# Optimization experiments

Hardware: AMD Instinct MI355X
Metric: run time of the kernel (lower is better)

The kernel has to match this reference:

```python
import jax, jax.numpy as jnp
import numpy as np

B, S, D, H, DH, TLEN, TD = 4, 1024, 1024, 16, 64, 256, 256
EPS = 1e-5


def layer_norm(x, g, b):
    m = jnp.mean(x, axis=-1, keepdims=True)
    v = jnp.mean((x - m) ** 2, axis=-1, keepdims=True)
    return (x - m) * jax.lax.rsqrt(v + EPS) * g + b


def rotate_half(x):
    x1, x2 = jnp.split(x, 2, axis=-1)
    return jnp.concatenate((-x2, x1), axis=-1)


def apply_rope(pos, t):
    # pos: [S, DH] -> [1, S, 1, DH]; t: [B, S, H, DH]
    p = pos[None, :, None, :]
    return t * jnp.cos(p) + rotate_half(t) * jnp.sin(p)


def mha(q_in, kv_in, in_w, in_b, out_w, out_b, n_heads):
    # standard nn.MultiheadAttention math (batch-first tensors here)
    d = q_in.shape[-1]
    dh = d // n_heads
    q = q_in @ in_w[:d].T + in_b[:d]
    k = kv_in @ in_w[d:2 * d].T + in_b[d:2 * d]
    v = kv_in @ in_w[2 * d:].T + in_b[2 * d:]
    q = q.reshape(q.shape[0], q.shape[1], n_heads, dh)
    k = k.reshape(k.shape[0], k.shape[1], n_heads, dh)
    v = v.reshape(v.shape[0], v.shape[1], n_heads, dh)
    scores = jnp.einsum('bihd,bjhd->bhij', q, k) / jnp.sqrt(jnp.asarray(dh, q.dtype))
    attn = jax.nn.softmax(scores, axis=-1)
    o = jnp.einsum('bhij,bjhd->bihd', attn, v)
    o = o.reshape(o.shape[0], o.shape[1], d)
    return o @ out_w.T + out_b


def setup_inputs():
    key = jax.random.key(0)
    ks = jax.random.split(key, 20)
    s = 0.02
    inp = {
        'x': jax.random.normal(ks[0], (B, S, D), jnp.float32),
        'text_emb': jax.random.normal(ks[1], (B, TLEN, D), jnp.float32),
        'time_emb': jax.random.normal(ks[2], (B, TD), jnp.float32),
    }
    # true RoPE position encoding, matching RotaryEmbedding.forward
    inv_freq = 1.0 / (10000 ** (jnp.arange(0, DH, 2, dtype=jnp.float32) / DH))
    freqs = jnp.arange(S, dtype=jnp.float32)[:, None] * inv_freq[None, :]
    inp['rotary_pos'] = jnp.concatenate((freqs, freqs), axis=-1)  # [S, DH]
    inp.update(
        ln1_g=jnp.ones((D,), jnp.float32), ln1_b=jnp.zeros((D,), jnp.float32),
        ln2_g=jnp.ones((D,), jnp.float32), ln2_b=jnp.zeros((D,), jnp.float32),
        ln3_g=jnp.ones((D,), jnp.float32), ln3_b=jnp.zeros((D,), jnp.float32),
        attn_in_w=jax.random.normal(ks[3], (3 * D, D), jnp.float32) * s,
        attn_in_b=jnp.zeros((3 * D,), jnp.float32),
        ca_in_w=jax.random.normal(ks[4], (3 * D, D), jnp.float32) * s,
        ca_in_b=jnp.zeros((3 * D,), jnp.float32),
        ca_out_w=jax.random.normal(ks[5], (D, D), jnp.float32) * s,
        ca_out_b=jnp.zeros((D,), jnp.float32),
        fc1_w=jax.random.normal(ks[6], (4 * D, D), jnp.float32) * s,
        fc1_b=jnp.zeros((4 * D,), jnp.float32),
        gate_w=jax.random.normal(ks[7], (4 * D, D), jnp.float32) * s,
        gate_b=jnp.zeros((4 * D,), jnp.float32),
        fc2_w=jax.random.normal(ks[8], (D, 4 * D), jnp.float32) * s,
        fc2_b=jnp.zeros((D,), jnp.float32),
    )
    return inp


def reference(x, text_emb, time_emb, rotary_pos,
              ln1_g, ln1_b, ln2_g, ln2_b, ln3_g, ln3_b,
              attn_in_w, attn_in_b,
              ca_in_w, ca_in_b, ca_out_w, ca_out_b,
              fc1_w, fc1_b, gate_w, gate_b, fc2_w, fc2_b):
    b, n, d = x.shape
    # --- self-attention with manual RoPE (NOTE: original skips out_proj) ---
    residual = x
    xn = layer_norm(x, ln1_g, ln1_b)
    q = xn @ attn_in_w[:d].T + attn_in_b[:d]
    k = xn @ attn_in_w[d:2 * d].T + attn_in_b[d:2 * d]
    v = xn @ attn_in_w[2 * d:].T + attn_in_b[2 * d:]
    q = q.reshape(b, n, H, DH)
    k = k.reshape(b, n, H, DH)
    v = v.reshape(b, n, H, DH)
    q = apply_rope(rotary_pos, q)
    k = apply_rope(rotary_pos, k)
    scores = jnp.einsum('bihd,bjhd->bhij', q, k) / jnp.sqrt(jnp.asarray(DH, x.dtype))
    attn = jax.nn.softmax(scores, axis=-1)
    attn_out = jnp.einsum('bhij,bjhd->bihd', attn, v).reshape(b, n, d)
    x = attn_out + residual
    # --- cross-attention (full MHA, dropout inactive at eval) ---
    residual = x
    xn = layer_norm(x, ln2_g, ln2_b)
    x = mha(xn, text_emb, ca_in_w, ca_in_b, ca_out_w, ca_out_b, H) + residual
    # --- gated MLP ---
    residual = x
    xn = layer_norm(x, ln3_g, ln3_b)
    h = jax.nn.gelu(xn @ fc1_w.T + fc1_b, approximate=False)
    g = jax.nn.sigmoid(xn @ gate_w.T + gate_b)
    return (h * g) @ fc2_w.T + fc2_b + residual
```

## Files before the change

kernel.cpp:

```cpp
#include <hip/hip_runtime.h>
#include <hip/hip_bf16.h>

#define SEQ 1024
#define DIM 1024
#define NH 16

typedef __bf16 bf16_t;
typedef __bf16 bf16x8 __attribute__((ext_vector_type(8)));
typedef __bf16 bf16x4 __attribute__((ext_vector_type(4)));
typedef float f32x4 __attribute__((ext_vector_type(4)));

__device__ __forceinline__ f32x4 mfma16(bf16x8 a, bf16x8 b, f32x4 c) {
    return __builtin_amdgcn_mfma_f32_16x16x32_bf16(a, b, c, 0, 0, 0);
}

__device__ __forceinline__ void gload16(const bf16_t* g, bf16_t* l) {
    __builtin_amdgcn_global_load_lds(
        (const __attribute__((address_space(1))) void*)g,
        (__attribute__((address_space(3))) void*)l, 16, 0, 0);
}

enum { EPI_BF16 = 0, EPI_F32_RESID = 1, EPI_BF16_GELU = 2, EPI_BF16_SIGMUL = 3 };

__global__ __launch_bounds__(256) void cvt_kernel(const float* __restrict__ in,
                                                  bf16_t* __restrict__ out) {
    const int i = blockIdx.x * 256 + threadIdx.x;
    const float4 v = ((const float4*)in)[i];
    bf16x4 o = {(bf16_t)v.x, (bf16_t)v.y, (bf16_t)v.z, (bf16_t)v.w};
    ((bf16x4*)out)[i] = o;
}

__global__ __launch_bounds__(256) void ln_kernel(const float* __restrict__ in,
                                                 const float* __restrict__ g,
                                                 const float* __restrict__ bsh,
                                                 bf16_t* __restrict__ out) {
    __shared__ float red[4], red2[4];
    const int row = blockIdx.x, tid = threadIdx.x;
    const float4 v = ((const float4*)(in + (size_t)row * DIM))[tid];
    float s = v.x + v.y + v.z + v.w;
#pragma unroll
    for (int o = 32; o; o >>= 1) s += __shfl_down(s, o, 64);
    if ((tid & 63) == 0) red[tid >> 6] = s;
    __syncthreads();
    const float mean = (red[0] + red[1] + red[2] + red[3]) * (1.0f / DIM);
    const float dx = v.x - mean, dy = v.y - mean, dz = v.z - mean, dw = v.w - mean;
    float s2 = dx * dx + dy * dy + dz * dz + dw * dw;
#pragma unroll
    for (int o = 32; o; o >>= 1) s2 += __shfl_xor(s2, o, 64);
    if ((tid & 63) == 0) red2[tid >> 6] = s2;
    __syncthreads();
    const float var = (red2[0] + red2[1] + red2[2] + red2[3]) * (1.0f / DIM);
    const float rs = rsqrtf(var + 1e-5f);
    const float4 gv = ((const float4*)g)[tid];
    const float4 bv = ((const float4*)bsh)[tid];
    bf16x4 o4 = {(bf16_t)(dx * rs * gv.x + bv.x), (bf16_t)(dy * rs * gv.y + bv.y),
                 (bf16_t)(dz * rs * gv.z + bv.z), (bf16_t)(dw * rs * gv.w + bv.w)};
    ((bf16x4*)(out + (size_t)row * DIM))[tid] = o4;
}

__global__ __launch_bounds__(256) void rope_kernel(bf16_t* __restrict__ qkv,
                                                   const float* __restrict__ rp) {
    const int t = blockIdx.x * 256 + threadIdx.x;
    const int row = t >> 9;
    const int rem = t & 511;
    const int h = rem >> 5, d = rem & 31;
    const int s = row & (SEQ - 1);
    const float p0 = rp[s * 64 + d];
    const float p1 = rp[s * 64 + d + 32];
    float s0, c0, s1, c1;
    sincosf(p0, &s0, &c0);
    sincosf(p1, &s1, &c1);
    const size_t base = (size_t)row * 3072 + h * 64 + d;
#pragma unroll
    for (int off = 0; off <= 1024; off += 1024) {
        const float a = (float)qkv[base + off];
        const float b = (float)qkv[base + off + 32];
        qkv[base + off] = (bf16_t)(a * c0 - b * s0);
        qkv[base + off + 32] = (bf16_t)(b * c1 + a * s1);
    }
}

__device__ __forceinline__ float epi_apply_gelu(float v) {
    return 0.5f * v * (1.0f + erff(v * 0.70710678118f));
}

__global__ __launch_bounds__(256) void vtrans_kernel(
    const bf16_t* __restrict__ src, int ld, int voff, int skv,
    bf16_t* __restrict__ vt) {
    __shared__ bf16_t T[64 * 72];
    const int qt = blockIdx.x, h = blockIdx.y, b = blockIdx.z;
    const int tid = threadIdx.x;
    const int s0 = qt * 64;
#pragma unroll
    for (int t = 0; t < 2; ++t) {
        const int idx = t * 256 + tid;
        const int r = idx >> 3, c8 = (idx & 7) * 8;
        bf16x8 v = *(const bf16x8*)(src + (size_t)(b * skv + s0 + r) * ld +
                                    voff + h * 64 + c8);
        *(bf16x8*)&T[r * 72 + c8] = v;
    }
    __syncthreads();
    const size_t base = ((size_t)(b * NH + h) * 64) * skv;
#pragma unroll
    for (int t = 0; t < 2; ++t) {
        const int idx = t * 256 + tid;
        const int d = idx >> 3, s8 = (idx & 7) * 8;
        bf16x8 w;
#pragma unroll
        for (int i = 0; i < 8; ++i) w[i] = T[(s8 + i) * 72 + d];
        *(bf16x8*)(vt + base + (size_t)d * skv + s0 + s8) = w;
    }
}

#define ALD 72
template <bool OUTBF>
__global__ __launch_bounds__(256) void attn2_kernel(
    const bf16_t* __restrict__ qp, int ldq, int qoff,
    const bf16_t* __restrict__ kp, int ldk, int koff,
    const bf16_t* __restrict__ vtp, int skv,
    const float* __restrict__ resid, void* __restrict__ outp, float scale) {
    __shared__ bf16_t Ks[4096];
    __shared__ bf16_t Vs[4096];
    __shared__ bf16_t Ps[4 * 16 * ALD];
    const int nwg = gridDim.x;
    const int t = (blockIdx.x & 7) * (nwg >> 3) + (blockIdx.x >> 3);
    const int qt = t & 15;
    const int bh = t >> 4;
    const int b = bh >> 4, h = bh & 15;
    const int tid = threadIdx.x;
    const int wave = tid >> 6, lane = tid & 63;
    const int lr = lane & 15, hi = lane >> 4;

    const size_t qrow = (size_t)(b * SEQ + qt * 64 + wave * 16 + lr);
    const bf16_t* qb = qp + qrow * ldq + qoff + h * 64;
    const bf16x8 qf0 = *(const bf16x8*)(qb + hi * 8);
    const bf16x8 qf1 = *(const bf16x8*)(qb + 32 + hi * 8);

    const bf16_t* vbase = vtp + ((size_t)bh * 64) * skv;

    f32x4 oacc[4];
#pragma unroll
    for (int n = 0; n < 4; ++n) oacc[n] = (f32x4){0.f, 0.f, 0.f, 0.f};
    float mrun[4] = {-1e30f, -1e30f, -1e30f, -1e30f};
    float lrun[4] = {0.f, 0.f, 0.f, 0.f};

    bf16_t* pw = &Ps[wave * 16 * ALD];
    const int nkt = skv >> 6;
    for (int kt = 0; kt < nkt; ++kt) {
#pragma unroll
        for (int u = 0; u < 2; ++u) {
            const int c = wave * 2 + u;
            const int grow = wave * 16 + lr, gcol = u * 32 + hi * 8;
            gload16(kp + (size_t)(b * skv + kt * 64 + grow) * ldk + koff +
                        h * 64 + gcol,
                    &Ks[c * 512]);
            gload16(vbase + (size_t)grow * skv + kt * 64 + gcol, &Vs[c * 512]);
        }
        __syncthreads();

        f32x4 s[4];
#pragma unroll
        for (int n = 0; n < 4; ++n) {
            f32x4 z = (f32x4){0.f, 0.f, 0.f, 0.f};
            z = mfma16(qf0, *(const bf16x8*)&Ks[(n * 2 + 0) * 512 + hi * 128 + lr * 8], z);
            z = mfma16(qf1, *(const bf16x8*)&Ks[(n * 2 + 1) * 512 + hi * 128 + lr * 8], z);
            s[n] = z * scale;
        }
        float alpha[4];
#pragma unroll
        for (int j = 0; j < 4; ++j) {
            float mt = fmaxf(fmaxf(s[0][j], s[1][j]), fmaxf(s[2][j], s[3][j]));
#pragma unroll
            for (int o = 8; o >= 1; o >>= 1) mt = fmaxf(mt, __shfl_xor(mt, o, 64));
            const float mnew = fmaxf(mrun[j], mt);
            alpha[j] = __expf(mrun[j] - mnew);
            float rsum = 0.f;
#pragma unroll
            for (int n = 0; n < 4; ++n) {
                const float p = __expf(s[n][j] - mnew);
                s[n][j] = p;
                rsum += p;
            }
#pragma unroll
            for (int o = 8; o >= 1; o >>= 1) rsum += __shfl_xor(rsum, o, 64);
            lrun[j] = lrun[j] * alpha[j] + rsum;
            mrun[j] = mnew;
        }
#pragma unroll
        for (int j = 0; j < 4; ++j) {
            const int pr = hi * 4 + j;
#pragma unroll
            for (int n = 0; n < 4; ++n) pw[pr * ALD + n * 16 + lr] = (bf16_t)s[n][j];
        }
#pragma unroll
        for (int n = 0; n < 4; ++n)
#pragma unroll
            for (int j = 0; j < 4; ++j) oacc[n][j] *= alpha[j];
#pragma unroll
        for (int ks = 0; ks < 2; ++ks) {
            const bf16x8 pa = *(const bf16x8*)&pw[lr * ALD + ks * 32 + hi * 8];
#pragma unroll
            for (int n = 0; n < 4; ++n) {
                const bf16x8 vf =
                    *(const bf16x8*)&Vs[(n * 2 + ks) * 512 + hi * 128 + lr * 8];
                oacc[n] = mfma16(pa, vf, oacc[n]);
            }
        }
        __syncthreads();
    }

    const size_t orow0 = (size_t)(b * SEQ + qt * 64 + wave * 16);
#pragma unroll
    for (int n = 0; n < 4; ++n) {
#pragma unroll
        for (int j = 0; j < 4; ++j) {
            const int r = hi * 4 + j;
            const size_t idx = (orow0 + r) * DIM + h * 64 + n * 16 + lr;
            float val = oacc[n][j] / lrun[j];
            if constexpr (OUTBF) {
                ((bf16_t*)outp)[idx] = (bf16_t)val;
            } else {
                ((float*)outp)[idx] = val + resid[idx];
            }
        }
    }
}

template <int EPI>
__global__ __launch_bounds__(512, 4) void gemm8w(
    const bf16_t* __restrict__ A, int lda, const bf16_t* __restrict__ W, int ldw,
    const float* __restrict__ bias, const void* __restrict__ aux,
    void* __restrict__ outv, int ldo, int K, int nM) {
    __shared__ bf16_t As[2][8192];
    __shared__ bf16_t Bs[2][8192];
    const int tid = threadIdx.x;
    const int wave = tid >> 6, lane = tid & 63;
    const int wm = wave >> 2, wn = wave & 3;
    const int lr = lane & 15, hi = lane >> 4;

    const int q = gridDim.x >> 3;
    const int t = (blockIdx.x & 7) * q + (blockIdx.x >> 3);
    const int rowA0 = (t % nM) * 128;
    const int rowB0 = (t / nM) * 128;

    f32x4 acc[4][2];
#pragma unroll
    for (int m = 0; m < 4; ++m)
#pragma unroll
        for (int n = 0; n < 2; ++n) acc[m][n] = (f32x4){0.f, 0.f, 0.f, 0.f};

    const int c0 = wave * 2;
    auto stage = [&](int kt, int b) {
        const int k0 = kt * 64;
#pragma unroll
        for (int u = 0; u < 2; ++u) {
            const int c = c0 + u, s = c >> 1, ks = c & 1;
            const int grow = s * 16 + lr, gcol = k0 + ks * 32 + hi * 8;
            gload16(A + (size_t)(rowA0 + grow) * lda + gcol, &As[b][c * 512]);
            gload16(W + (size_t)(rowB0 + grow) * ldw + gcol, &Bs[b][c * 512]);
        }
    };

    const int NT = K >> 6;
    stage(0, 0);
    __syncthreads();

    for (int kt = 0; kt < NT; ++kt) {
        const int cur = kt & 1;
        if (kt + 1 < NT) stage(kt + 1, cur ^ 1);
#pragma unroll
        for (int ks = 0; ks < 2; ++ks) {
            bf16x8 af[4], bfr[2];
#pragma unroll
            for (int mf = 0; mf < 4; ++mf)
                af[mf] = *(const bf16x8*)&As[cur][((wm * 4 + mf) * 2 + ks) * 512 +
                                                 hi * 128 + lr * 8];
#pragma unroll
            for (int nf = 0; nf < 2; ++nf)
                bfr[nf] = *(const bf16x8*)&Bs[cur][((wn * 2 + nf) * 2 + ks) * 512 +
                                                  hi * 128 + lr * 8];
#pragma unroll
            for (int mf = 0; mf < 4; ++mf)
#pragma unroll
                for (int nf = 0; nf < 2; ++nf)
                    acc[mf][nf] = mfma16(af[mf], bfr[nf], acc[mf][nf]);
        }
        __syncthreads();
    }

    float bn[2];
#pragma unroll
    for (int n = 0; n < 2; ++n) bn[n] = bias[rowB0 + wn * 32 + n * 16 + lr];
#pragma unroll
    for (int m = 0; m < 4; ++m) {
#pragma unroll
        for (int j = 0; j < 4; ++j) {
            const int row = rowA0 + wm * 64 + m * 16 + hi * 4 + j;
#pragma unroll
            for (int n = 0; n < 2; ++n) {
                const int col = rowB0 + wn * 32 + n * 16 + lr;
                float val = acc[m][n][j] + bn[n];
                const size_t oidx = (size_t)row * ldo + col;
                if constexpr (EPI == EPI_BF16) {
                    ((bf16_t*)outv)[oidx] = (bf16_t)val;
                } else if constexpr (EPI == EPI_F32_RESID) {
                    ((float*)outv)[oidx] = val + ((const float*)aux)[oidx];
                } else if constexpr (EPI == EPI_BF16_GELU) {
                    ((bf16_t*)outv)[oidx] = (bf16_t)epi_apply_gelu(val);
                } else {
                    const float sg = 1.0f / (1.0f + expf(-val));
                    ((bf16_t*)outv)[oidx] =
                        (bf16_t)(sg * (float)((const bf16_t*)aux)[oidx]);
                }
            }
        }
    }
}

extern "C" void kernel_launch(void* const* d_in, const int* in_sizes, int n_in,
                              void* d_out, int out_size, void* d_ws, size_t ws_size,
                              hipStream_t stream) {
    const float* x = (const float*)d_in[0];
    const float* text_emb = (const float*)d_in[1];
    const float* rotary = (const float*)d_in[3];
    const float* ln1_g = (const float*)d_in[4];
    const float* ln1_b = (const float*)d_in[5];
    const float* ln2_g = (const float*)d_in[6];
    const float* ln2_b = (const float*)d_in[7];
    const float* ln3_g = (const float*)d_in[8];
    const float* ln3_b = (const float*)d_in[9];
    const float* attn_in_w = (const float*)d_in[10];
    const float* attn_in_b = (const float*)d_in[11];
    const float* ca_in_w = (const float*)d_in[12];
    const float* ca_in_b = (const float*)d_in[13];
    const float* ca_out_w = (const float*)d_in[14];
    const float* ca_out_b = (const float*)d_in[15];
    const float* fc1_w = (const float*)d_in[16];
    const float* fc1_b = (const float*)d_in[17];
    const float* gate_w = (const float*)d_in[18];
    const float* gate_b = (const float*)d_in[19];
    const float* fc2_w = (const float*)d_in[20];
    const float* fc2_b = (const float*)d_in[21];

    char* ws = (char*)d_ws;
    bf16_t* attn_w_bf = (bf16_t*)(ws);
    bf16_t* ca_in_bf = (bf16_t*)(ws + 6291456);
    bf16_t* ca_out_bf = (bf16_t*)(ws + 12582912);
    bf16_t* fc1_bf = (bf16_t*)(ws + 14680064);
    bf16_t* gate_bf = (bf16_t*)(ws + 23068672);
    bf16_t* fc2_bf = (bf16_t*)(ws + 31457280);
    bf16_t* text_bf = (bf16_t*)(ws + 39845888);
    bf16_t* xn = (bf16_t*)(ws + 41943040);
    float* xA = (float*)(ws + 50331648);
    char* S = ws + 67108864;
    bf16_t* qkv = (bf16_t*)S;
    bf16_t* vtSelf = (bf16_t*)(S + 25165824);
    bf16_t* cq = (bf16_t*)S;
    bf16_t* ckv = (bf16_t*)(S + 8388608);
    bf16_t* ca_attn = (bf16_t*)(S + 12582912);
    bf16_t* vtCross = (bf16_t*)(S + 20971520);
    bf16_t* hbuf = (bf16_t*)S;
    float* out = (float*)d_out;

    cvt_kernel<<<3072, 256, 0, stream>>>(attn_in_w, attn_w_bf);
    cvt_kernel<<<3072, 256, 0, stream>>>(ca_in_w, ca_in_bf);
    cvt_kernel<<<1024, 256, 0, stream>>>(ca_out_w, ca_out_bf);
    cvt_kernel<<<4096, 256, 0, stream>>>(fc1_w, fc1_bf);
    cvt_kernel<<<4096, 256, 0, stream>>>(gate_w, gate_bf);
    cvt_kernel<<<4096, 256, 0, stream>>>(fc2_w, fc2_bf);
    cvt_kernel<<<1024, 256, 0, stream>>>(text_emb, text_bf);

    ln_kernel<<<4096, 256, 0, stream>>>(x, ln1_g, ln1_b, xn);
    gemm8w<EPI_BF16><<<768, 512, 0, stream>>>(
        xn, 1024, attn_w_bf, 1024, attn_in_b, nullptr, qkv, 3072, 1024, 32);
    rope_kernel<<<8192, 256, 0, stream>>>(qkv, rotary);
    vtrans_kernel<<<dim3(16, 16, 4), 256, 0, stream>>>(qkv, 3072, 2048, 1024, vtSelf);
    attn2_kernel<false><<<1024, 256, 0, stream>>>(
        qkv, 3072, 0, qkv, 3072, 1024, vtSelf, 1024, x, xA, 0.125f);

    ln_kernel<<<4096, 256, 0, stream>>>(xA, ln2_g, ln2_b, xn);
    gemm8w<EPI_BF16><<<256, 512, 0, stream>>>(
        xn, 1024, ca_in_bf, 1024, ca_in_b, nullptr, cq, 1024, 1024, 32);
    gemm8w<EPI_BF16><<<128, 512, 0, stream>>>(
        text_bf, 1024, ca_in_bf + (size_t)1024 * 1024, 1024, ca_in_b + 1024, nullptr,
        ckv, 2048, 1024, 8);
    vtrans_kernel<<<dim3(4, 16, 4), 256, 0, stream>>>(ckv, 2048, 1024, 256, vtCross);
    attn2_kernel<true><<<1024, 256, 0, stream>>>(
        cq, 1024, 0, ckv, 2048, 0, vtCross, 256, nullptr, ca_attn, 0.125f);
    gemm8w<EPI_F32_RESID><<<256, 512, 0, stream>>>(
        ca_attn, 1024, ca_out_bf, 1024, ca_out_b, xA, xA, 1024, 1024, 32);

    ln_kernel<<<4096, 256, 0, stream>>>(xA, ln3_g, ln3_b, xn);
    gemm8w<EPI_BF16_GELU><<<1024, 512, 0, stream>>>(
        xn, 1024, fc1_bf, 1024, fc1_b, nullptr, hbuf, 4096, 1024, 32);
    gemm8w<EPI_BF16_SIGMUL><<<1024, 512, 0, stream>>>(
        xn, 1024, gate_bf, 1024, gate_b, hbuf, hbuf, 4096, 1024, 32);
    gemm8w<EPI_F32_RESID><<<256, 512, 0, stream>>>(
        hbuf, 4096, fc2_bf, 4096, fc2_b, xA, out, 1024, 4096, 32);
}
```

Baseline: 534.4 us.

## Fuse fc1 and gate GEMMs, pipeline GEMM loads, remap block-to-XCD tiles

Adds a gemm_mlp kernel that computes the fc1 and gate projections in one pass over a 128x64 output tile. Each wave loads its B rows from either the fc1 or the gate weights, and the epilogue applies GELU times sigmoid directly. This removes the bf16 round trip of the intermediate h through hbuf and the second read of xn. The GEMM main loop now prefetches two k-tiles ahead, using explicit vmcnt waits and raw barriers in place of __syncthreads. The block-index swizzle is also rewritten so that blocks sharing M or N tiles land on the same XCD (MODE selects which), aiming at better L2 reuse. The fused kernel uses narrower N tiles and launches twice as many blocks.

```diff
diff --git a/kernel.cpp b/kernel.cpp
--- a/kernel.cpp
+++ b/kernel.cpp
@@ -20,7 +20,7 @@
         (__attribute__((address_space(3))) void*)l, 16, 0, 0);
 }
 
-enum { EPI_BF16 = 0, EPI_F32_RESID = 1, EPI_BF16_GELU = 2, EPI_BF16_SIGMUL = 3 };
+enum { EPI_BF16 = 0, EPI_F32_RESID = 1 };
 
 __global__ __launch_bounds__(256) void cvt_kernel(const float* __restrict__ in,
                                                   bf16_t* __restrict__ out) {
@@ -226,7 +226,7 @@
     }
 }
 
-template <int EPI>
+template <int EPI, int MODE>
 __global__ __launch_bounds__(512, 4) void gemm8w(
     const bf16_t* __restrict__ A, int lda, const bf16_t* __restrict__ W, int ldw,
     const float* __restrict__ bias, const void* __restrict__ aux,
@@ -238,10 +238,18 @@
     const int wm = wave >> 2, wn = wave & 3;
     const int lr = lane & 15, hi = lane >> 4;
 
-    const int q = gridDim.x >> 3;
-    const int t = (blockIdx.x & 7) * q + (blockIdx.x >> 3);
-    const int rowA0 = (t % nM) * 128;
-    const int rowB0 = (t / nM) * 128;
+    const int x = blockIdx.x & 7, i = blockIdx.x >> 3;
+    int mt, nt;
+    if constexpr (MODE == 0) {
+        const int mc = nM >> 3;
+        mt = x * mc + (i % mc);
+        nt = i / mc;
+    } else {
+        const int nc = (gridDim.x / nM) >> 3;
+        nt = x * nc + (i % nc);
+        mt = i / nc;
+    }
+    const int rowA0 = mt * 128, rowB0 = nt * 128;
 
     f32x4 acc[4][2];
 #pragma unroll
@@ -249,13 +257,12 @@
 #pragma unroll
         for (int n = 0; n < 2; ++n) acc[m][n] = (f32x4){0.f, 0.f, 0.f, 0.f};
 
-    const int c0 = wave * 2;
     auto stage = [&](int kt, int b) {
         const int k0 = kt * 64;
 #pragma unroll
         for (int u = 0; u < 2; ++u) {
-            const int c = c0 + u, s = c >> 1, ks = c & 1;
-            const int grow = s * 16 + lr, gcol = k0 + ks * 32 + hi * 8;
+            const int c = wave * 2 + u;
+            const int grow = wave * 16 + lr, gcol = k0 + u * 32 + hi * 8;
             gload16(A + (size_t)(rowA0 + grow) * lda + gcol, &As[b][c * 512]);
             gload16(W + (size_t)(rowB0 + grow) * ldw + gcol, &Bs[b][c * 512]);
         }
@@ -263,11 +270,12 @@
 
     const int NT = K >> 6;
     stage(0, 0);
-    __syncthreads();
+    stage(1, 1);
+    asm volatile("s_waitcnt vmcnt(4)" ::: "memory");
+    __builtin_amdgcn_s_barrier();
 
     for (int kt = 0; kt < NT; ++kt) {
         const int cur = kt & 1;
-        if (kt + 1 < NT) stage(kt + 1, cur ^ 1);
 #pragma unroll
         for (int ks = 0; ks < 2; ++ks) {
             bf16x8 af[4], bfr[2];
@@ -285,7 +293,17 @@
                 for (int nf = 0; nf < 2; ++nf)
                     acc[mf][nf] = mfma16(af[mf], bfr[nf], acc[mf][nf]);
         }
-        __syncthreads();
+        if (kt + 1 < NT) {
+            __builtin_amdgcn_sched_barrier(0);
+            __builtin_amdgcn_s_barrier();
+            if (kt + 2 < NT) {
+                stage(kt + 2, cur);
+                asm volatile("s_waitcnt vmcnt(4)" ::: "memory");
+            } else {
+                asm volatile("s_waitcnt vmcnt(0)" ::: "memory");
+            }
+            __builtin_amdgcn_s_barrier();
+        }
     }
 
     float bn[2];
@@ -303,16 +321,98 @@
                 const size_t oidx = (size_t)row * ldo + col;
                 if constexpr (EPI == EPI_BF16) {
                     ((bf16_t*)outv)[oidx] = (bf16_t)val;
-                } else if constexpr (EPI == EPI_F32_RESID) {
+                } else {
                     ((float*)outv)[oidx] = val + ((const float*)aux)[oidx];
-                } else if constexpr (EPI == EPI_BF16_GELU) {
-                    ((bf16_t*)outv)[oidx] = (bf16_t)epi_apply_gelu(val);
-                } else {
-                    const float sg = 1.0f / (1.0f + expf(-val));
-                    ((bf16_t*)outv)[oidx] =
-                        (bf16_t)(sg * (float)((const bf16_t*)aux)[oidx]);
                 }
             }
+        }
+    }
+}
+
+__global__ __launch_bounds__(512, 4) void gemm_mlp(
+    const bf16_t* __restrict__ A, int lda, const bf16_t* __restrict__ W1,
+    const bf16_t* __restrict__ Wg, int ldw, const float* __restrict__ b1,
+    const float* __restrict__ bg, bf16_t* __restrict__ outv, int ldo, int K,
+    int nM) {
+    __shared__ bf16_t As[2][8192];
+    __shared__ bf16_t Bs[2][8192];
+    const int tid = threadIdx.x;
+    const int wave = tid >> 6, lane = tid & 63;
+    const int wm = wave >> 2, wn = wave & 3;
+    const int lr = lane & 15, hi = lane >> 4;
+
+    const int x = blockIdx.x & 7, i = blockIdx.x >> 3;
+    const int nc = (gridDim.x / nM) >> 3;
+    const int nt = x * nc + (i % nc), mt = i / nc;
+    const int rowA0 = mt * 128, colB0 = nt * 64;
+
+    f32x4 acc[4][2];
+#pragma unroll
+    for (int m = 0; m < 4; ++m)
+#pragma unroll
+        for (int n = 0; n < 2; ++n) acc[m][n] = (f32x4){0.f, 0.f, 0.f, 0.f};
+
+    const bf16_t* Wsrc = (wave & 1) ? Wg : W1;
+    const int wrow = colB0 + (wave >> 1) * 16 + lr;
+    auto stage = [&](int kt, int b) {
+        const int k0 = kt * 64;
+#pragma unroll
+        for (int u = 0; u < 2; ++u) {
+            const int c = wave * 2 + u;
+            const int gcol = k0 + u * 32 + hi * 8;
+            gload16(A + (size_t)(rowA0 + wave * 16 + lr) * lda + gcol,
+                    &As[b][c * 512]);
+            gload16(Wsrc + (size_t)wrow * ldw + gcol, &Bs[b][c * 512]);
+        }
+    };
+
+    const int NT = K >> 6;
+    stage(0, 0);
+    stage(1, 1);
+    asm volatile("s_waitcnt vmcnt(4)" ::: "memory");
+    __builtin_amdgcn_s_barrier();
+
+    for (int kt = 0; kt < NT; ++kt) {
+        const int cur = kt & 1;
+#pragma unroll
+        for (int ks = 0; ks < 2; ++ks) {
+            bf16x8 af[4], bh, bg_;
+#pragma unroll
+            for (int mf = 0; mf < 4; ++mf)
+                af[mf] = *(const bf16x8*)&As[cur][((wm * 4 + mf) * 2 + ks) * 512 +
+                                                 hi * 128 + lr * 8];
+            bh = *(const bf16x8*)&Bs[cur][((2 * wn) * 2 + ks) * 512 + hi * 128 + lr * 8];
+            bg_ = *(const bf16x8*)&Bs[cur][((2 * wn + 1) * 2 + ks) * 512 + hi * 128 + lr * 8];
+#pragma unroll
+            for (int mf = 0; mf < 4; ++mf) {
+                acc[mf][0] = mfma16(af[mf], bh, acc[mf][0]);
+                acc[mf][1] = mfma16(af[mf], bg_, acc[mf][1]);
+            }
+        }
+        if (kt + 1 < NT) {
+            __builtin_amdgcn_sched_barrier(0);
+            __builtin_amdgcn_s_barrier();
+            if (kt + 2 < NT) {
+                stage(kt + 2, cur);
+                asm volatile("s_waitcnt vmcnt(4)" ::: "memory");
+            } else {
+                asm volatile("s_waitcnt vmcnt(0)" ::: "memory");
+            }
+            __builtin_amdgcn_s_barrier();
+        }
+    }
+
+    const int col = colB0 + wn * 16 + lr;
+    const float bb1 = b1[col], bbg = bg[col];
+#pragma unroll
+    for (int m = 0; m < 4; ++m) {
+#pragma unroll
+        for (int j = 0; j < 4; ++j) {
+            const int row = rowA0 + wm * 64 + m * 16 + hi * 4 + j;
+            const float h = acc[m][0][j] + bb1;
+            const float g = acc[m][1][j] + bbg;
+            const float sg = 1.0f / (1.0f + __expf(-g));
+            outv[(size_t)row * ldo + col] = (bf16_t)(epi_apply_gelu(h) * sg);
         }
     }
 }
@@ -371,7 +471,7 @@
     cvt_kernel<<<1024, 256, 0, stream>>>(text_emb, text_bf);
 
     ln_kernel<<<4096, 256, 0, stream>>>(x, ln1_g, ln1_b, xn);
-    gemm8w<EPI_BF16><<<768, 512, 0, stream>>>(
+    gemm8w<EPI_BF16, 0><<<768, 512, 0, stream>>>(
         xn, 1024, attn_w_bf, 1024, attn_in_b, nullptr, qkv, 3072, 1024, 32);
     rope_kernel<<<8192, 256, 0, stream>>>(qkv, rotary);
     vtrans_kernel<<<dim3(16, 16, 4), 256, 0, stream>>>(qkv, 3072, 2048, 1024, vtSelf);
@@ -379,22 +479,20 @@
         qkv, 3072, 0, qkv, 3072, 1024, vtSelf, 1024, x, xA, 0.125f);
 
     ln_kernel<<<4096, 256, 0, stream>>>(xA, ln2_g, ln2_b, xn);
-    gemm8w<EPI_BF16><<<256, 512, 0, stream>>>(
+    gemm8w<EPI_BF16, 0><<<256, 512, 0, stream>>>(
         xn, 1024, ca_in_bf, 1024, ca_in_b, nullptr, cq, 1024, 1024, 32);
-    gemm8w<EPI_BF16><<<128, 512, 0, stream>>>(
+    gemm8w<EPI_BF16, 1><<<128, 512, 0, stream>>>(
         text_bf, 1024, ca_in_bf + (size_t)1024 * 1024, 1024, ca_in_b + 1024, nullptr,
         ckv, 2048, 1024, 8);
     vtrans_kernel<<<dim3(4, 16, 4), 256, 0, stream>>>(ckv, 2048, 1024, 256, vtCross);
     attn2_kernel<true><<<1024, 256, 0, stream>>>(
         cq, 1024, 0, ckv, 2048, 0, vtCross, 256, nullptr, ca_attn, 0.125f);
-    gemm8w<EPI_F32_RESID><<<256, 512, 0, stream>>>(
+    gemm8w<EPI_F32_RESID, 0><<<256, 512, 0, stream>>>(
         ca_attn, 1024, ca_out_bf, 1024, ca_out_b, xA, xA, 1024, 1024, 32);
 
     ln_kernel<<<4096, 256, 0, stream>>>(xA, ln3_g, ln3_b, xn);
-    gemm8w<EPI_BF16_GELU><<<1024, 512, 0, stream>>>(
-        xn, 1024, fc1_bf, 1024, fc1_b, nullptr, hbuf, 4096, 1024, 32);
-    gemm8w<EPI_BF16_SIGMUL><<<1024, 512, 0, stream>>>(
-        xn, 1024, gate_bf, 1024, gate_b, hbuf, hbuf, 4096, 1024, 32);
-    gemm8w<EPI_F32_RESID><<<256, 512, 0, stream>>>(
+    gemm_mlp<<<2048, 512, 0, stream>>>(
+        xn, 1024, fc1_bf, gate_bf, 1024, fc1_b, gate_b, hbuf, 4096, 1024, 32);
+    gemm8w<EPI_F32_RESID, 0><<<256, 512, 0, stream>>>(
         hbuf, 4096, fc2_bf, 4096, fc2_b, xA, out, 1024, 4096, 32);
 }
```

After: 512.5 us. -4.1%, faster.
